# Performance work log

Measured on AMD Instinct MI355X. Metric: run time of the kernel, lower is better.

Reference implementation:

```python
import jax, jax.numpy as jnp
import numpy as np

B, T, L = 256, 2048, 48  # batch, seq_len, nb_labels


def setup_inputs() -> dict:
    key = jax.random.key(0)
    k1, k2, k3 = jax.random.split(key, 3)
    emissions = jax.random.normal(k1, (B, T, L), dtype=jnp.float32)
    tags = jax.random.randint(k2, (B, T), 0, L, dtype=jnp.int32)
    # matches nn.init.uniform_(transitions, -0.1, 0.1)
    transitions = jax.random.uniform(k3, (L, L), dtype=jnp.float32, minval=-0.1, maxval=0.1)
    return {"emissions": emissions, "tags": tags, "transitions": transitions}


def _gold_scores(emissions, tags, transitions):
    # emission score at every gold tag: [B, T] -> sum over T
    e = jnp.take_along_axis(emissions, tags[..., None], axis=2)[..., 0].sum(axis=1)
    # transition scores between consecutive gold tags
    t = transitions[tags[:, :-1], tags[:, 1:]].sum(axis=1)
    start = transitions[0, tags[:, 0]]      # row 0 acts as start scores
    end = transitions[tags[:, -1], -1]      # last column acts as end scores
    return e + t + start + end              # [B]


def _log_partition(emissions, transitions):
    # forward algorithm: alpha_t[b, j] = logsumexp_i(alpha_{t-1}[b, i] + T[i, j]) + em[b, t, j]
    alpha0 = transitions[0][None, :] + emissions[:, 0]          # [B, L]
    em_rest = jnp.moveaxis(emissions[:, 1:], 1, 0)              # [T-1, B, L]

    def step(alpha, em_t):
        alpha = jax.nn.logsumexp(alpha[:, :, None] + transitions[None, :, :], axis=1) + em_t
        return alpha, None

    alpha, _ = jax.lax.scan(step, alpha0, em_rest)
    return jax.nn.logsumexp(alpha + transitions[:, -1][None, :], axis=1)  # [B]


def reference(emissions, tags, transitions):
    """neg_log_likelihood of LinearChainCRF: -sum(scores - log_partition)."""
    scores = _gold_scores(emissions, tags, transitions)
    partition = _log_partition(emissions, transitions)
    return -jnp.sum(scores - partition)
```

## Files before the change

kernel.cpp:

```cpp
#include <hip/hip_runtime.h>

#define B 256
#define T 2048
#define L 48
#define G 16
#define SEG 128
#define KNORM 4.371f
#define TOTALF (B * T * L)

typedef short v4s __attribute__((ext_vector_type(4)));
typedef short v8s __attribute__((ext_vector_type(8)));
typedef float v4f __attribute__((ext_vector_type(4)));
typedef int   v2i __attribute__((ext_vector_type(2)));

#define WAVE_SYNC() asm volatile("s_waitcnt lgkmcnt(0)" ::: "memory")

#if __has_builtin(__builtin_amdgcn_mfma_f32_16x16x16bf16_1k)
#define MFMA16(a, b, c) __builtin_amdgcn_mfma_f32_16x16x16bf16_1k((a), (b), (c), 0, 0, 0)
#else
__device__ __forceinline__ v4f mfma16_asm(v4s a, v4s b, v4f c) {
    asm volatile("v_mfma_f32_16x16x16_bf16 %0, %1, %2, %0\n\ts_nop 7\n\ts_nop 7"
                 : "+v"(c) : "v"(a), "v"(b));
    return c;
}
#define MFMA16(a, b, c) mfma16_asm((a), (b), (c))
#endif

#if __has_builtin(__builtin_amdgcn_mfma_f32_16x16x32_bf16)
typedef __bf16 v8y __attribute__((ext_vector_type(8)));
__device__ __forceinline__ v4f mfma32(v8s a, v8s b, v4f c) {
    return __builtin_amdgcn_mfma_f32_16x16x32_bf16(
        __builtin_bit_cast(v8y, a), __builtin_bit_cast(v8y, b), c, 0, 0, 0);
}
#else
__device__ __forceinline__ v4f mfma32(v8s a, v8s b, v4f c) {
    asm volatile("v_mfma_f32_16x16x32_bf16 %0, %1, %2, %0\n\ts_nop 7\n\ts_nop 7"
                 : "+v"(c) : "v"(a), "v"(b));
    return c;
}
#endif

__device__ __forceinline__ unsigned cvt_pk(float lo, float hi) {
    unsigned r;
    asm("v_cvt_pk_bf16_f32 %0, %1, %2" : "=v"(r) : "v"(lo), "v"(hi));
    return r;
}

__device__ __forceinline__ v4s scale_pack(v4f cf, v4f g) {
    v4f a = cf * g;
    v2i d;
    d.x = (int)cvt_pk(a.x, a.y);
    d.y = (int)cvt_pk(a.z, a.w);
    return __builtin_bit_cast(v4s, d);
}

__global__ __launch_bounds__(192, 6) void crf_scan(
    const float* __restrict__ em, const int* __restrict__ tags,
    const float* __restrict__ trans, float* __restrict__ out,
    float* __restrict__ ws)
{
    const int b   = blockIdx.x >> 4;
    const int s   = blockIdx.x & 15;
    const int tid = threadIdx.x;
    const int ct  = tid >> 6;
    const int ln  = tid & 63;
    const int q   = ln >> 4;
    const int c   = ln & 15;

    __shared__ __align__(16) float smem[2 * 384];

    const size_t bem = (size_t)b * T * L;
    const int t0 = 1 + SEG * s;
    const int t1 = (t0 + SEG < T) ? (t0 + SEG) : T;

    v8s A32[3];
    #pragma unroll
    for (int rt = 0; rt < 3; ++rt) {
        const int m = 16 * rt + c;
        uint4 aw;
        aw.x = cvt_pk(__expf(trans[(4 * q + 0) * L + m]),
                      __expf(trans[(4 * q + 1) * L + m]));
        aw.y = cvt_pk(__expf(trans[(4 * q + 2) * L + m]),
                      __expf(trans[(4 * q + 3) * L + m]));
        aw.z = cvt_pk(__expf(trans[(16 + 4 * q + 0) * L + m]),
                      __expf(trans[(16 + 4 * q + 1) * L + m]));
        aw.w = cvt_pk(__expf(trans[(16 + 4 * q + 2) * L + m]),
                      __expf(trans[(16 + 4 * q + 3) * L + m]));
        A32[rt] = __builtin_bit_cast(v8s, aw);
    }
    v4s A16[3];
    #pragma unroll
    for (int rt = 0; rt < 3; ++rt) {
        const int m = 16 * rt + c;
        v2i d;
        d.x = (int)cvt_pk(__expf(trans[(32 + 4 * q + 0) * L + m]),
                          __expf(trans[(32 + 4 * q + 1) * L + m]));
        d.y = (int)cvt_pk(__expf(trans[(32 + 4 * q + 2) * L + m]),
                          __expf(trans[(32 + 4 * q + 3) * L + m]));
        A16[rt] = __builtin_bit_cast(v4s, d);
    }

    const int col = 16 * ct + c;
    v8s Bq01;
    v4s Bq2;
    {
        int4 w;
        w.x = (4 * q + 0 == col ? 0x3F80 : 0) | (4 * q + 1 == col ? 0x3F800000 : 0);
        w.y = (4 * q + 2 == col ? 0x3F80 : 0) | (4 * q + 3 == col ? 0x3F800000 : 0);
        w.z = (16 + 4 * q + 0 == col ? 0x3F80 : 0) | (16 + 4 * q + 1 == col ? 0x3F800000 : 0);
        w.w = (16 + 4 * q + 2 == col ? 0x3F80 : 0) | (16 + 4 * q + 3 == col ? 0x3F800000 : 0);
        Bq01 = __builtin_bit_cast(v8s, w);
        v2i d2;
        d2.x = (32 + 4 * q + 0 == col ? 0x3F80 : 0) | (32 + 4 * q + 1 == col ? 0x3F800000 : 0);
        d2.y = (32 + 4 * q + 2 == col ? 0x3F80 : 0) | (32 + 4 * q + 3 == col ? 0x3F800000 : 0);
        Bq2 = __builtin_bit_cast(v4s, d2);
    }

    const v4f zero4 = {0.f, 0.f, 0.f, 0.f};

    auto do_step = [&](const float* rowp) {
        v4f gv[3];
        #pragma unroll
        for (int rt = 0; rt < 3; ++rt)
            gv[rt] = *(const v4f*)(rowp + 16 * rt + 4 * q);
        v4f Cf[3];
        #pragma unroll
        for (int rt = 0; rt < 3; ++rt) {
            v4f acc = mfma32(A32[rt], Bq01, zero4);
            Cf[rt] = MFMA16(A16[rt], Bq2, acc);
        }
        v4s n0 = scale_pack(Cf[0], gv[0]);
        v4s n1 = scale_pack(Cf[1], gv[1]);
        v2i a_ = __builtin_bit_cast(v2i, n0);
        v2i b_ = __builtin_bit_cast(v2i, n1);
        int4 fw; fw.x = a_.x; fw.y = a_.y; fw.z = b_.x; fw.w = b_.y;
        Bq01 = __builtin_bit_cast(v8s, fw);
        Bq2  = scale_pack(Cf[2], gv[2]);
    };

    {
        size_t gf = bem + (size_t)t0 * L;
        smem[tid]       = __expf(em[gf + tid]       - KNORM);
        smem[tid + 192] = __expf(em[gf + tid + 192] - KNORM);
        __syncthreads();
    }

    for (int bk = 0; bk < 16; ++bk) {
        const float* cur = smem + (bk & 1) * 384;
        float* nxt = smem + ((bk & 1) ^ 1) * 384;

        size_t gf = bem + (size_t)(t0 + 8 * (bk + 1)) * L;
        if (gf > (size_t)TOTALF - 384) gf = (size_t)TOTALF - 384;
        float stg0 = em[gf + tid];
        float stg1 = em[gf + tid + 192];

        #pragma unroll
        for (int k = 0; k < 8; ++k)
            if (t0 + 8 * bk + k < t1)
                do_step(cur + 48 * k);

        nxt[tid]       = __expf(stg0 - KNORM);
        nxt[tid + 192] = __expf(stg1 - KNORM);
        __syncthreads();
    }

    unsigned short* qs = (unsigned short*)ws + (size_t)(b * G + s) * 2304;
    v2i dt[3];
    {
        int4 w01 = __builtin_bit_cast(int4, Bq01);
        dt[0].x = w01.x; dt[0].y = w01.y;
        dt[1].x = w01.z; dt[1].y = w01.w;
        dt[2] = __builtin_bit_cast(v2i, Bq2);
    }
    #pragma unroll
    for (int kt = 0; kt < 3; ++kt) {
        v2i d = dt[kt];
        int r0 = 16 * kt + 4 * q;
        qs[(r0 + 0) * 48 + col] = (unsigned short)((unsigned)d.x & 0xffffu);
        qs[(r0 + 1) * 48 + col] = (unsigned short)((unsigned)d.x >> 16);
        qs[(r0 + 2) * 48 + col] = (unsigned short)((unsigned)d.y & 0xffffu);
        qs[(r0 + 3) * 48 + col] = (unsigned short)((unsigned)d.y >> 16);
    }

    const int* tg = tags + (size_t)b * T;
    float gp = 0.f;
    if (tid < 128) {
        int t = SEG * s + tid;
        int tag = tg[t];
        gp += em[bem + (size_t)t * L + tag];
        if (t < T - 1)  gp += trans[tag * L + tg[t + 1]];
        if (t == 0)     gp += trans[tag];
        if (t == T - 1) gp += trans[tag * L + (L - 1)];
    }
    #pragma unroll
    for (int off = 32; off; off >>= 1) gp += __shfl_xor(gp, off);
    __shared__ float red[3];
    if (ln == 0) red[ct] = gp;
    __syncthreads();
    if (tid == 0) atomicAdd(out, -(red[0] + red[1] + red[2]));
}

__global__ __launch_bounds__(64) void crf_combine(
    const float* __restrict__ em, const float* __restrict__ trans,
    const float* __restrict__ ws, float* __restrict__ out)
{
    const int b = blockIdx.x, l = threadIdx.x;
    const int lc = (l < L) ? l : (L - 1);

    __shared__ float us[64];

    const unsigned short* qb = (const unsigned short*)ws + (size_t)b * G * 2304;

    float u = (l < L) ? __expf(trans[l] + em[(size_t)b * T * L + l]) : 0.f;
    float logtot = 2047.0f * KNORM;

    uint4 pre[6];
    {
        const uint4* p = (const uint4*)(qb + lc * 48);
        #pragma unroll
        for (int ii = 0; ii < 6; ++ii) pre[ii] = p[ii];
    }

    for (int s = 0; s < G; ++s) {
        us[l] = u;
        uint4 cur[6];
        #pragma unroll
        for (int ii = 0; ii < 6; ++ii) cur[ii] = pre[ii];
        if (s + 1 < G) {
            const uint4* p = (const uint4*)(qb + (size_t)(s + 1) * 2304 + lc * 48);
            #pragma unroll
            for (int ii = 0; ii < 6; ++ii) pre[ii] = p[ii];
        }
        WAVE_SYNC();

        float acc = 0.f;
        #pragma unroll
        for (int ii = 0; ii < 6; ++ii) {
            unsigned w0 = cur[ii].x, w1 = cur[ii].y, w2 = cur[ii].z, w3 = cur[ii].w;
            int jj = ii * 8;
            acc = fmaf(__uint_as_float(w0 << 16),          us[jj + 0], acc);
            acc = fmaf(__uint_as_float(w0 & 0xffff0000u),  us[jj + 1], acc);
            acc = fmaf(__uint_as_float(w1 << 16),          us[jj + 2], acc);
            acc = fmaf(__uint_as_float(w1 & 0xffff0000u),  us[jj + 3], acc);
            acc = fmaf(__uint_as_float(w2 << 16),          us[jj + 4], acc);
            acc = fmaf(__uint_as_float(w2 & 0xffff0000u),  us[jj + 5], acc);
            acc = fmaf(__uint_as_float(w3 << 16),          us[jj + 6], acc);
            acc = fmaf(__uint_as_float(w3 & 0xffff0000u),  us[jj + 7], acc);
        }
        WAVE_SYNC();

        float r = __int_as_float(
            __builtin_amdgcn_readlane(__float_as_int(acc), 0));
        logtot += __logf(r);
        u = (l < L) ? acc * __builtin_amdgcn_rcpf(r) : 0.f;
    }

    float v = (l < L) ? u * __expf(trans[lc * L + (L - 1)]) : 0.f;
    #pragma unroll
    for (int off = 32; off; off >>= 1) v += __shfl_xor(v, off);
    if (l == 0) atomicAdd(out, logtot + __logf(v));
}

extern "C" void kernel_launch(void* const* d_in, const int* in_sizes, int n_in,
                              void* d_out, int out_size, void* d_ws, size_t ws_size,
                              hipStream_t stream) {
    const float* em    = (const float*)d_in[0];
    const int*   tags  = (const int*)  d_in[1];
    const float* trans = (const float*)d_in[2];
    float* out = (float*)d_out;
    float* ws  = (float*)d_ws;

    (void)hipMemsetAsync(out, 0, sizeof(float), stream);
    crf_scan   <<<B * G, 192, 0, stream>>>(em, tags, trans, out, ws);
    crf_combine<<<B,      64, 0, stream>>>(em, trans, ws, out);
}
```

Measured before the change: 262.0 us.

## Interleave two independent segment chains per block to hide MFMA latency

Each block now processes two time segments (s and s+8) of the same batch row, interleaving their dependent MFMA chains so one chain's matrix ops can fill the latency of the other. Grid size is halved, shared-memory staging is doubled, and the gold-path scoring loops over both segments. This trades occupancy and register pressure for more instruction-level parallelism in the serial recurrence.

```diff
diff --git a/kernel.cpp b/kernel.cpp
--- a/kernel.cpp
+++ b/kernel.cpp
@@ -54,24 +54,31 @@
     return __builtin_bit_cast(v4s, d);
 }
 
+__device__ __forceinline__ v8s fuse01(v4s n0, v4s n1) {
+    v2i a_ = __builtin_bit_cast(v2i, n0);
+    v2i b_ = __builtin_bit_cast(v2i, n1);
+    int4 fw; fw.x = a_.x; fw.y = a_.y; fw.z = b_.x; fw.w = b_.y;
+    return __builtin_bit_cast(v8s, fw);
+}
+
 __global__ __launch_bounds__(192, 6) void crf_scan(
     const float* __restrict__ em, const int* __restrict__ tags,
     const float* __restrict__ trans, float* __restrict__ out,
     float* __restrict__ ws)
 {
-    const int b   = blockIdx.x >> 4;
-    const int s   = blockIdx.x & 15;
+    const int b   = blockIdx.x >> 3;
+    const int s   = blockIdx.x & 7;
     const int tid = threadIdx.x;
     const int ct  = tid >> 6;
     const int ln  = tid & 63;
     const int q   = ln >> 4;
     const int c   = ln & 15;
 
-    __shared__ __align__(16) float smem[2 * 384];
+    __shared__ __align__(16) float smem[2 * 768];
 
     const size_t bem = (size_t)b * T * L;
-    const int t0 = 1 + SEG * s;
-    const int t1 = (t0 + SEG < T) ? (t0 + SEG) : T;
+    const int t0A = 1 + SEG * s;
+    const int t0B = 1 + SEG * (s + 8);
 
     v8s A32[3];
     #pragma unroll
@@ -101,96 +108,130 @@
     }
 
     const int col = 16 * ct + c;
-    v8s Bq01;
-    v4s Bq2;
+    v8s BqA01, BqB01;
+    v4s BqA2, BqB2;
     {
         int4 w;
         w.x = (4 * q + 0 == col ? 0x3F80 : 0) | (4 * q + 1 == col ? 0x3F800000 : 0);
         w.y = (4 * q + 2 == col ? 0x3F80 : 0) | (4 * q + 3 == col ? 0x3F800000 : 0);
         w.z = (16 + 4 * q + 0 == col ? 0x3F80 : 0) | (16 + 4 * q + 1 == col ? 0x3F800000 : 0);
         w.w = (16 + 4 * q + 2 == col ? 0x3F80 : 0) | (16 + 4 * q + 3 == col ? 0x3F800000 : 0);
-        Bq01 = __builtin_bit_cast(v8s, w);
+        BqA01 = __builtin_bit_cast(v8s, w);
+        BqB01 = BqA01;
         v2i d2;
         d2.x = (32 + 4 * q + 0 == col ? 0x3F80 : 0) | (32 + 4 * q + 1 == col ? 0x3F800000 : 0);
         d2.y = (32 + 4 * q + 2 == col ? 0x3F80 : 0) | (32 + 4 * q + 3 == col ? 0x3F800000 : 0);
-        Bq2 = __builtin_bit_cast(v4s, d2);
+        BqA2 = __builtin_bit_cast(v4s, d2);
+        BqB2 = BqA2;
     }
 
     const v4f zero4 = {0.f, 0.f, 0.f, 0.f};
 
-    auto do_step = [&](const float* rowp) {
-        v4f gv[3];
-        #pragma unroll
-        for (int rt = 0; rt < 3; ++rt)
-            gv[rt] = *(const v4f*)(rowp + 16 * rt + 4 * q);
-        v4f Cf[3];
-        #pragma unroll
-        for (int rt = 0; rt < 3; ++rt) {
-            v4f acc = mfma32(A32[rt], Bq01, zero4);
-            Cf[rt] = MFMA16(A16[rt], Bq2, acc);
-        }
-        v4s n0 = scale_pack(Cf[0], gv[0]);
-        v4s n1 = scale_pack(Cf[1], gv[1]);
-        v2i a_ = __builtin_bit_cast(v2i, n0);
-        v2i b_ = __builtin_bit_cast(v2i, n1);
-        int4 fw; fw.x = a_.x; fw.y = a_.y; fw.z = b_.x; fw.w = b_.y;
-        Bq01 = __builtin_bit_cast(v8s, fw);
-        Bq2  = scale_pack(Cf[2], gv[2]);
+    auto do_step2 = [&](const float* rpA, const float* rpB, bool commitB) {
+        v4f a0 = mfma32(A32[0], BqA01, zero4);
+        v4f b0 = mfma32(A32[0], BqB01, zero4);
+        v4f a1 = mfma32(A32[1], BqA01, zero4);
+        v4f b1 = mfma32(A32[1], BqB01, zero4);
+        v4f a2 = mfma32(A32[2], BqA01, zero4);
+        v4f b2 = mfma32(A32[2], BqB01, zero4);
+        a0 = MFMA16(A16[0], BqA2, a0);
+        b0 = MFMA16(A16[0], BqB2, b0);
+        a1 = MFMA16(A16[1], BqA2, a1);
+        b1 = MFMA16(A16[1], BqB2, b1);
+        a2 = MFMA16(A16[2], BqA2, a2);
+        b2 = MFMA16(A16[2], BqB2, b2);
+
+        v4f gA0 = *(const v4f*)(rpA + 4 * q);
+        v4f gA1 = *(const v4f*)(rpA + 16 + 4 * q);
+        v4f gA2 = *(const v4f*)(rpA + 32 + 4 * q);
+        BqA01 = fuse01(scale_pack(a0, gA0), scale_pack(a1, gA1));
+        BqA2  = scale_pack(a2, gA2);
+
+        v4f gB0 = *(const v4f*)(rpB + 4 * q);
+        v4f gB1 = *(const v4f*)(rpB + 16 + 4 * q);
+        v4f gB2 = *(const v4f*)(rpB + 32 + 4 * q);
+        v4s nB0 = scale_pack(b0, gB0);
+        v4s nB1 = scale_pack(b1, gB1);
+        v4s nB2 = scale_pack(b2, gB2);
+        if (commitB) {
+            BqB01 = fuse01(nB0, nB1);
+            BqB2  = nB2;
+        }
     };
 
     {
-        size_t gf = bem + (size_t)t0 * L;
-        smem[tid]       = __expf(em[gf + tid]       - KNORM);
-        smem[tid + 192] = __expf(em[gf + tid + 192] - KNORM);
+        size_t gfA = bem + (size_t)t0A * L;
+        size_t gfB = bem + (size_t)t0B * L;
+        smem[tid]             = __expf(em[gfA + tid]       - KNORM);
+        smem[tid + 192]       = __expf(em[gfA + tid + 192] - KNORM);
+        smem[384 + tid]       = __expf(em[gfB + tid]       - KNORM);
+        smem[384 + tid + 192] = __expf(em[gfB + tid + 192] - KNORM);
         __syncthreads();
     }
 
     for (int bk = 0; bk < 16; ++bk) {
-        const float* cur = smem + (bk & 1) * 384;
-        float* nxt = smem + ((bk & 1) ^ 1) * 384;
-
-        size_t gf = bem + (size_t)(t0 + 8 * (bk + 1)) * L;
-        if (gf > (size_t)TOTALF - 384) gf = (size_t)TOTALF - 384;
-        float stg0 = em[gf + tid];
-        float stg1 = em[gf + tid + 192];
-
-        #pragma unroll
-        for (int k = 0; k < 8; ++k)
-            if (t0 + 8 * bk + k < t1)
-                do_step(cur + 48 * k);
-
-        nxt[tid]       = __expf(stg0 - KNORM);
-        nxt[tid + 192] = __expf(stg1 - KNORM);
+        const float* cur = smem + (bk & 1) * 768;
+        float* nxt = smem + ((bk & 1) ^ 1) * 768;
+
+        size_t gfA = bem + (size_t)(t0A + 8 * (bk + 1)) * L;
+        size_t gfB = bem + (size_t)(t0B + 8 * (bk + 1)) * L;
+        if (gfB > (size_t)TOTALF - 384) gfB = (size_t)TOTALF - 384;
+        float sA0 = em[gfA + tid];
+        float sA1 = em[gfA + tid + 192];
+        float sB0 = em[gfB + tid];
+        float sB1 = em[gfB + tid + 192];
+
+        #pragma unroll
+        for (int k = 0; k < 8; ++k) {
+            bool commitB = (t0B + 8 * bk + k < T);
+            do_step2(cur + 48 * k, cur + 384 + 48 * k, commitB);
+        }
+
+        nxt[tid]             = __expf(sA0 - KNORM);
+        nxt[tid + 192]       = __expf(sA1 - KNORM);
+        nxt[384 + tid]       = __expf(sB0 - KNORM);
+        nxt[384 + tid + 192] = __expf(sB1 - KNORM);
         __syncthreads();
     }
 
-    unsigned short* qs = (unsigned short*)ws + (size_t)(b * G + s) * 2304;
-    v2i dt[3];
     {
-        int4 w01 = __builtin_bit_cast(int4, Bq01);
-        dt[0].x = w01.x; dt[0].y = w01.y;
-        dt[1].x = w01.z; dt[1].y = w01.w;
-        dt[2] = __builtin_bit_cast(v2i, Bq2);
-    }
-    #pragma unroll
-    for (int kt = 0; kt < 3; ++kt) {
-        v2i d = dt[kt];
-        int r0 = 16 * kt + 4 * q;
-        qs[(r0 + 0) * 48 + col] = (unsigned short)((unsigned)d.x & 0xffffu);
-        qs[(r0 + 1) * 48 + col] = (unsigned short)((unsigned)d.x >> 16);
-        qs[(r0 + 2) * 48 + col] = (unsigned short)((unsigned)d.y & 0xffffu);
-        qs[(r0 + 3) * 48 + col] = (unsigned short)((unsigned)d.y >> 16);
+        unsigned short* qsA = (unsigned short*)ws + (size_t)(b * G + s) * 2304;
+        unsigned short* qsB = (unsigned short*)ws + (size_t)(b * G + s + 8) * 2304;
+        int4 wA = __builtin_bit_cast(int4, BqA01);
+        int4 wB = __builtin_bit_cast(int4, BqB01);
+        v2i dA2 = __builtin_bit_cast(v2i, BqA2);
+        v2i dB2 = __builtin_bit_cast(v2i, BqB2);
+        int rows[3] = {4 * q, 16 + 4 * q, 32 + 4 * q};
+        int aw[3][2] = {{wA.x, wA.y}, {wA.z, wA.w}, {dA2.x, dA2.y}};
+        int bw[3][2] = {{wB.x, wB.y}, {wB.z, wB.w}, {dB2.x, dB2.y}};
+        #pragma unroll
+        for (int kt = 0; kt < 3; ++kt) {
+            int r0 = rows[kt];
+            unsigned x = (unsigned)aw[kt][0], y = (unsigned)aw[kt][1];
+            qsA[(r0 + 0) * 48 + col] = (unsigned short)(x & 0xffffu);
+            qsA[(r0 + 1) * 48 + col] = (unsigned short)(x >> 16);
+            qsA[(r0 + 2) * 48 + col] = (unsigned short)(y & 0xffffu);
+            qsA[(r0 + 3) * 48 + col] = (unsigned short)(y >> 16);
+            x = (unsigned)bw[kt][0]; y = (unsigned)bw[kt][1];
+            qsB[(r0 + 0) * 48 + col] = (unsigned short)(x & 0xffffu);
+            qsB[(r0 + 1) * 48 + col] = (unsigned short)(x >> 16);
+            qsB[(r0 + 2) * 48 + col] = (unsigned short)(y & 0xffffu);
+            qsB[(r0 + 3) * 48 + col] = (unsigned short)(y >> 16);
+        }
     }
 
     const int* tg = tags + (size_t)b * T;
     float gp = 0.f;
     if (tid < 128) {
-        int t = SEG * s + tid;
-        int tag = tg[t];
-        gp += em[bem + (size_t)t * L + tag];
-        if (t < T - 1)  gp += trans[tag * L + tg[t + 1]];
-        if (t == 0)     gp += trans[tag];
-        if (t == T - 1) gp += trans[tag * L + (L - 1)];
+        #pragma unroll
+        for (int hh = 0; hh < 2; ++hh) {
+            int t = SEG * (s + 8 * hh) + tid;
+            int tag = tg[t];
+            gp += em[bem + (size_t)t * L + tag];
+            if (t < T - 1)  gp += trans[tag * L + tg[t + 1]];
+            if (t == 0)     gp += trans[tag];
+            if (t == T - 1) gp += trans[tag * L + (L - 1)];
+        }
     }
     #pragma unroll
     for (int off = 32; off; off >>= 1) gp += __shfl_xor(gp, off);
@@ -271,6 +312,6 @@
     float* ws  = (float*)d_ws;
 
     (void)hipMemsetAsync(out, 0, sizeof(float), stream);
-    crf_scan   <<<B * G, 192, 0, stream>>>(em, tags, trans, out, ws);
-    crf_combine<<<B,      64, 0, stream>>>(em, trans, ws, out);
-}
+    crf_scan   <<<B * 8, 192, 0, stream>>>(em, tags, trans, out, ws);
+    crf_combine<<<B,     64, 0, stream>>>(em, trans, ws, out);
+}
```

Result: slower. 272.3 us (+3.9%).
